# Kernel optimization log

Hardware: AMD Instinct MI355X
Metric: run time of the kernel (lower is better)

The kernel has to match this reference:

```python
import jax, jax.numpy as jnp
import numpy as np

B, S_T, S_S, P, D = 4, 8, 4, 1024, 1024
NUM_REF = 256
NUM_SHARED = 256
TOPK = 4
TEMP = 1.0
STUDENT_FRAMES = [0, 2, 4, 6]          # teacher indices used by student
EXTRA_FRAMES = [1, 3, 5, 7]            # teacher-only frames
SHARED_TEACHER = [2, 4, 6]             # shared frames (student_frame_indices[1:])
W_D1 = W_D2 = W_D3 = 1.0
HUBER_OUTER_BETA = 0.5


def setup_inputs() -> dict:
    key = jax.random.key(0)
    k1, k2, k3, k4 = jax.random.split(key, 4)
    teacher_feats = jax.random.normal(k1, (B, S_T, P, D), dtype=jnp.float32)
    student_feats = jax.random.normal(k2, (B, S_S, P, D), dtype=jnp.float32)
    ref_perm = jax.random.randint(k3, (NUM_REF,), 0, P, dtype=jnp.int32)
    shared_perm = jax.random.randint(k4, (NUM_SHARED,), 0, P, dtype=jnp.int32)
    return {"teacher_feats": teacher_feats, "student_feats": student_feats,
            "ref_perm": ref_perm, "shared_perm": shared_perm}


def _l2_normalize(x, eps=1e-12):
    n = jnp.maximum(jnp.linalg.norm(x, axis=-1, keepdims=True), eps)
    return x / n


def _smooth_l1_zero(x, beta):
    # SmoothL1Loss(x, 0) elementwise
    ax = jnp.abs(x)
    return jnp.where(ax < beta, 0.5 * ax * ax / beta, ax - 0.5 * beta)


def _kl_branch(diff_t, diff_s):
    # KL(softmax(diff_t/T) || softmax(diff_s/T)) over last dim, then outer huber vs 0
    log_p = jax.nn.log_softmax(diff_t / TEMP, axis=-1)
    log_q = jax.nn.log_softmax(diff_s / TEMP, axis=-1)
    kl = jnp.sum(jnp.exp(log_p) * (log_p - log_q), axis=-1)
    return jnp.sum(_smooth_l1_zero(kl, HUBER_OUTER_BETA)), kl.size


def reference(teacher_feats, student_feats, ref_perm, shared_perm):
    sg = jax.lax.stop_gradient
    N = min(NUM_REF, NUM_SHARED)

    # ref frame (teacher idx 0 -> student idx 0), subsampled patches
    ref_t = sg(teacher_feats[:, 0][:, ref_perm, :])          # [B, num_ref, D]
    ref_s = student_feats[:, 0][:, ref_perm, :]

    # teacher-only frames concatenated along patch dim: [B, 4*P, D]
    extra_t = sg(teacher_feats[:, jnp.array(EXTRA_FRAMES)].reshape(B, len(EXTRA_FRAMES) * P, D))

    # cosine-similarity top-k search (selection_mode='topk')
    sim = jnp.einsum('bnd,bmd->bnm', _l2_normalize(ref_t), _l2_normalize(extra_t))
    _, topk_idx = jax.lax.top_k(sim, TOPK)                    # [B, num_ref, topk]
    sim_high = jax.vmap(lambda e, i: e[i])(extra_t, topk_idx)  # [B, num_ref, topk, D]
    sim_high = sg(sim_high)

    rt = ref_t[:, :N, :]
    rs = ref_s[:, :N, :]
    sh = sim_high[:, :N, :, :]

    sum_d1 = jnp.float32(0.0); sum_d2 = jnp.float32(0.0); sum_d3 = jnp.float32(0.0)
    n_d1 = 0; n_d2 = 0; n_d3 = 0

    for t_idx in SHARED_TEACHER:
        s_idx = STUDENT_FRAMES.index(t_idx)
        st = sg(teacher_feats[:, t_idx][:, shared_perm[:N], :])   # [B, N, D]
        ss = student_feats[:, s_idx][:, shared_perm[:N], :]

        # d1: ref - shared
        l1, c1 = _kl_branch(rt - st, rs - ss)
        sum_d1 += l1; n_d1 += c1
        # d2: ref - sim_high
        l2, c2 = _kl_branch(rt[:, :, None, :] - sh, rs[:, :, None, :] - sh)
        sum_d2 += l2; n_d2 += c2
        # d3: shared - sim_high
        l3, c3 = _kl_branch(st[:, :, None, :] - sh, ss[:, :, None, :] - sh)
        sum_d3 += l3; n_d3 += c3

    loss = (W_D1 * sum_d1 / n_d1 + W_D2 * sum_d2 / n_d2 + W_D3 * sum_d3 / n_d3)
    return loss
```

## Files before the change

### kernel.cpp

```cpp
#include <hip/hip_runtime.h>
#include <hip/hip_bf16.h>
#include <math.h>

#define BATCH 4

typedef __bf16 bf16x8 __attribute__((ext_vector_type(8)));
typedef float f32x4 __attribute__((ext_vector_type(4)));

#define LDSTRIDE 40

__global__ __launch_bounds__(256) void convert_kernel(const float* __restrict__ teacher,
                                                      const int* __restrict__ ref_perm,
                                                      __bf16* __restrict__ Abf,
                                                      __bf16* __restrict__ Bbf,
                                                      float* __restrict__ invnorm,
                                                      float* __restrict__ acc) {
    int blk = blockIdx.x;
    int b = blk / 4352;
    int r = blk - b * 4352;
    int t = threadIdx.x;
    if (blk == 0 && t < 4) acc[t] = 0.f;
    const float* src;
    __bf16* dst;
    bool isB = (r >= 256);
    if (!isB) {
        src = teacher + (((size_t)b * 8 + 0) * 1024 + ref_perm[r]) * 1024;
        dst = Abf + ((size_t)b * 256 + r) * 1024;
    } else {
        int m = r - 256;
        int frame = 1 + 2 * (m >> 10), p = m & 1023;
        src = teacher + (((size_t)b * 8 + frame) * 1024 + p) * 1024;
        dst = Bbf + ((size_t)b * 4096 + m) * 1024;
    }
    float4 v = ((const float4*)src)[t];
    float scale = 1.0f;
    __shared__ float red[4];
    if (isB) {
        float s = v.x * v.x + v.y * v.y + v.z * v.z + v.w * v.w;
        for (int o = 32; o > 0; o >>= 1) s += __shfl_xor(s, o);
        if ((t & 63) == 0) red[t >> 6] = s;
        __syncthreads();
        float tot = red[0] + red[1] + red[2] + red[3];
        scale = 1.0f / fmaxf(sqrtf(tot), 1e-12f);
        if (t == 0) invnorm[b * 4096 + (r - 256)] = scale;
    }
    __bf16 o4[4] = {(__bf16)(v.x * scale), (__bf16)(v.y * scale),
                    (__bf16)(v.z * scale), (__bf16)(v.w * scale)};
    ((uint2*)dst)[t] = *(uint2*)o4;
}

__global__ __launch_bounds__(512) void mfma_gemm_kernel(const __bf16* __restrict__ Abf,
                                                        const __bf16* __restrict__ Bbf,
                                                        __bf16* __restrict__ scoresb) {
    int mt = blockIdx.x;
    int nt = blockIdx.y;
    int b  = blockIdx.z;
    int t = threadIdx.x;
    int lane = t & 63, wave = t >> 6;
    int wn0 = (wave & 1) * 64;
    int wm0 = (wave >> 1) * 32;
    int l15 = lane & 15, l4 = lane >> 4;

    __shared__ __bf16 As[128 * LDSTRIDE];
    __shared__ __bf16 Bs[128 * LDSTRIDE];

    const __bf16* Ab = Abf + ((size_t)b * 256 + nt * 128) * 1024;
    const __bf16* Bb = Bbf + ((size_t)b * 4096 + mt * 128) * 1024;

    int row0 = t >> 2, kc0 = t & 3;

    f32x4 acc[4][2] = {};

    for (int k0 = 0; k0 < 1024; k0 += 32) {
        uint4 a0 = *(const uint4*)(Ab + (size_t)row0 * 1024 + k0 + kc0 * 8);
        uint4 b0 = *(const uint4*)(Bb + (size_t)row0 * 1024 + k0 + kc0 * 8);
        __syncthreads();
        *(uint4*)(As + row0 * LDSTRIDE + kc0 * 8) = a0;
        *(uint4*)(Bs + row0 * LDSTRIDE + kc0 * 8) = b0;
        __syncthreads();
        bf16x8 af[4], bfr[2];
#pragma unroll
        for (int i = 0; i < 4; i++)
            af[i] = *(const bf16x8*)(As + (wn0 + i * 16 + l15) * LDSTRIDE + l4 * 8);
#pragma unroll
        for (int j = 0; j < 2; j++)
            bfr[j] = *(const bf16x8*)(Bs + (wm0 + j * 16 + l15) * LDSTRIDE + l4 * 8);
#pragma unroll
        for (int i = 0; i < 4; i++)
#pragma unroll
            for (int j = 0; j < 2; j++)
                acc[i][j] = __builtin_amdgcn_mfma_f32_16x16x32_bf16(af[i], bfr[j], acc[i][j], 0, 0, 0);
    }

    __bf16* outp = scoresb + ((size_t)b * 256 + nt * 128) * 4096 + (size_t)mt * 128;
#pragma unroll
    for (int i = 0; i < 4; i++)
#pragma unroll
        for (int j = 0; j < 2; j++)
#pragma unroll
            for (int r = 0; r < 4; r++) {
                int n = wn0 + i * 16 + l4 * 4 + r;
                int m = wm0 + j * 16 + l15;
                outp[(size_t)n * 4096 + m] = (__bf16)acc[i][j][r];
            }
}

__global__ __launch_bounds__(256) void topk_kl_kernel(const __bf16* __restrict__ scoresb,
                                                      const float* __restrict__ teacher,
                                                      const float* __restrict__ student,
                                                      const int* __restrict__ ref_perm,
                                                      const int* __restrict__ shared_perm,
                                                      const float* __restrict__ invnorm,
                                                      float* __restrict__ acc) {
    int row = blockIdx.x;
    int b = row >> 8, n = row & 255;
    int t = threadIdx.x;
    int lane = t & 63, wave = t >> 6;

    __shared__ float rt[1024], rs[1024], st[1024], ss[1024];
    __shared__ float sh8[8][1024];
    __shared__ float cval[32];
    __shared__ int cidx[32];
    __shared__ int cand_i[8];
    __shared__ float exact_v[8];
    __shared__ int wslot[4];
    __shared__ float res3[3];
    if (t < 3) res3[t] = 0.f;

    const float* Tb = teacher + (size_t)b * 8 * 1024 * 1024;
    const float* Sb = student + (size_t)b * 4 * 1024 * 1024;

    int rp = ref_perm[n];
    ((float4*)rt)[t] = ((const float4*)(Tb + (size_t)rp * 1024))[t];
    ((float4*)rs)[t] = ((const float4*)(Sb + (size_t)rp * 1024))[t];

    const __bf16* srow = scoresb + (size_t)row * 4096;
    __bf16 xs[16];
    *(uint4*)xs = ((const uint4*)srow)[2 * t];
    *(uint4*)(xs + 8) = ((const uint4*)srow)[2 * t + 1];

    float v[8]; int ix[8];
#pragma unroll
    for (int i = 0; i < 8; i++) { v[i] = -1e38f; ix[i] = -1; }
#pragma unroll
    for (int jj = 0; jj < 16; jj++) {
        float xv = (float)xs[jj]; int xm = t * 16 + jj;
        if (xv > v[7]) {
            v[7] = xv; ix[7] = xm;
#pragma unroll
            for (int i = 7; i > 0; i--)
                if (v[i] > v[i - 1]) {
                    float tv = v[i]; v[i] = v[i - 1]; v[i - 1] = tv;
                    int ti = ix[i]; ix[i] = ix[i - 1]; ix[i - 1] = ti;
                }
        }
    }
    for (int r = 0; r < 8; r++) {
        float bv = v[0]; int bi = ix[0];
        for (int o = 32; o > 0; o >>= 1) {
            float ov = __shfl_xor(bv, o); int oi = __shfl_xor(bi, o);
            if (ov > bv || (ov == bv && oi > bi)) { bv = ov; bi = oi; }
        }
        if (lane == 0) { cval[wave * 8 + r] = bv; cidx[wave * 8 + r] = bi; }
        if (bi == ix[0]) {
            v[0] = v[1]; ix[0] = ix[1];
            v[1] = v[2]; ix[1] = ix[2];
            v[2] = v[3]; ix[2] = ix[3];
            v[3] = v[4]; ix[3] = ix[4];
            v[4] = v[5]; ix[4] = ix[5];
            v[5] = v[6]; ix[5] = ix[6];
            v[6] = v[7]; ix[6] = ix[7];
            v[7] = -1e38f; ix[7] = -1;
        }
    }
    __syncthreads();
    if (wave == 0) {
        float mv = (lane < 32) ? cval[lane] : -1e38f;
        int mi = (lane < 32) ? cidx[lane] : -1;
        for (int r = 0; r < 8; r++) {
            float bv = mv; int bi = mi;
            for (int o = 32; o > 0; o >>= 1) {
                float ov = __shfl_xor(bv, o); int oi = __shfl_xor(bi, o);
                if (ov > bv || (ov == bv && oi > bi)) { bv = ov; bi = oi; }
            }
            if (lane == 0) cand_i[r] = bi;
            if (bi == mi) mv = -1e38f;
        }
    }
    __syncthreads();
#pragma unroll
    for (int c = 0; c < 8; c++) {
        int m = cand_i[c];
        int frame = 1 + 2 * (m >> 10), p = m & 1023;
        ((float4*)sh8[c])[t] = ((const float4*)(Tb + ((size_t)frame * 1024 + p) * 1024))[t];
    }
    __syncthreads();
    for (int c = wave; c < 8; c += 4) {
        float s = 0.f;
#pragma unroll
        for (int jj = 0; jj < 16; jj++) {
            int d = lane + 64 * jj;
            s = fmaf(rt[d], sh8[c][d], s);
        }
        for (int o = 32; o > 0; o >>= 1) s += __shfl_xor(s, o);
        if (lane == 0) exact_v[c] = s * invnorm[b * 4096 + cand_i[c]];
    }
    __syncthreads();
    if (t == 0) {
        unsigned used = 0;
        for (int r = 0; r < 4; r++) {
            float bv = -1e38f; int bc = 0;
            for (int c = 0; c < 8; c++)
                if (!(used & (1u << c)) && exact_v[c] > bv) { bv = exact_v[c]; bc = c; }
            used |= 1u << bc;
            wslot[r] = bc;
        }
    }
    __syncthreads();
    const float* shp[4] = {sh8[wslot[0]], sh8[wslot[1]], sh8[wslot[2]], sh8[wslot[3]]};

    int sp = shared_perm[n];
    for (int ti = 0; ti < 3; ti++) {
        int t_idx = 2 * ti + 2;
        int s_idx = ti + 1;
        __syncthreads();
        ((float4*)st)[t] = ((const float4*)(Tb + ((size_t)t_idx * 1024 + sp) * 1024))[t];
        ((float4*)ss)[t] = ((const float4*)(Sb + ((size_t)s_idx * 1024 + sp) * 1024))[t];
        __syncthreads();

        for (int r = wave; r < 9; r += 4) {
            const float *At, *Bt, *Asx, *Bsx;
            int branch;
            if (r == 0)      { At = rt; Bt = st;         Asx = rs; Bsx = ss;         branch = 0; }
            else if (r < 5)  { At = rt; Bt = shp[r - 1]; Asx = rs; Bsx = shp[r - 1]; branch = 1; }
            else             { At = st; Bt = shp[r - 5]; Asx = ss; Bsx = shp[r - 5]; branch = 2; }

            float dt[16], ds[16];
            float mt = -1e38f, ms = -1e38f;
#pragma unroll
            for (int j = 0; j < 16; j++) {
                int d = lane + 64 * j;
                dt[j] = At[d] - Bt[d];
                ds[j] = Asx[d] - Bsx[d];
                mt = fmaxf(mt, dt[j]);
                ms = fmaxf(ms, ds[j]);
            }
            for (int o = 32; o > 0; o >>= 1) {
                mt = fmaxf(mt, __shfl_xor(mt, o));
                ms = fmaxf(ms, __shfl_xor(ms, o));
            }
            float Zt = 0.f, Zs = 0.f, Tn = 0.f;
#pragma unroll
            for (int j = 0; j < 16; j++) {
                float et = __expf(dt[j] - mt);
                Zt += et;
                Zs += __expf(ds[j] - ms);
                Tn += et * (dt[j] - ds[j]);
            }
            for (int o = 32; o > 0; o >>= 1) {
                Zt += __shfl_xor(Zt, o);
                Zs += __shfl_xor(Zs, o);
                Tn += __shfl_xor(Tn, o);
            }
            if (lane == 0) {
                float kl = Tn / Zt - mt - __logf(Zt) + ms + __logf(Zs);
                float ax = fabsf(kl);
                float h = ax < 0.5f ? ax * ax : ax - 0.25f;
                atomicAdd(&res3[branch], h);
            }
        }
    }
    __syncthreads();
    if (t < 3) atomicAdd(&acc[t], res3[t]);
}

__global__ void finalize_kernel(const float* __restrict__ acc, float* __restrict__ out) {
    out[0] = acc[0] / 3072.f + acc[1] / 12288.f + acc[2] / 12288.f;
}

extern "C" void kernel_launch(void* const* d_in, const int* in_sizes, int n_in,
                              void* d_out, int out_size, void* d_ws, size_t ws_size,
                              hipStream_t stream) {
    const float* teacher = (const float*)d_in[0];
    const float* student = (const float*)d_in[1];
    const int* ref_perm = (const int*)d_in[2];
    const int* shared_perm = (const int*)d_in[3];
    float* out = (float*)d_out;

    char* ws = (char*)d_ws;
    float* acc     = (float*)ws;
    float* invnorm = (float*)(ws + 64);
    __bf16* Abf    = (__bf16*)(ws + 64 + 65536 + 16384);
    __bf16* Bbf    = Abf + (size_t)4 * 256 * 1024;
    __bf16* scoresb = Bbf + (size_t)4 * 4096 * 1024;

    convert_kernel<<<BATCH * 4352, 256, 0, stream>>>(teacher, ref_perm, Abf, Bbf, invnorm, acc);
    mfma_gemm_kernel<<<dim3(32, 2, 4), 512, 0, stream>>>(Abf, Bbf, scoresb);
    topk_kl_kernel<<<1024, 256, 0, stream>>>(scoresb, teacher, student, ref_perm, shared_perm, invnorm, acc);
    finalize_kernel<<<1, 1, 0, stream>>>(acc, out);
}
```

Before: 293.4 us.

## Split top-k rescoring and KL into separate kernels with per-frame grid

Splits the fused top-k/KL kernel into a rescoring kernel that writes top-4 indices to workspace, and a KL kernel launched over (row, shared frame) for three times more blocks. The d2 branch is computed once per row (in ti==0 blocks) and weighted by 3 because it does not depend on the shared frame. The rescoring step now reads candidate rows straight from global memory instead of staging all 8 in LDS. This shrinks LDS per block and raises parallelism, in exchange for an extra launch, reloading the ref and sim_high rows in every frame block, and uneven work across ti blocks.

```diff
diff --git a/kernel.cpp b/kernel.cpp
--- a/kernel.cpp
+++ b/kernel.cpp
@@ -105,34 +105,25 @@
             }
 }
 
-__global__ __launch_bounds__(256) void topk_kl_kernel(const __bf16* __restrict__ scoresb,
-                                                      const float* __restrict__ teacher,
-                                                      const float* __restrict__ student,
-                                                      const int* __restrict__ ref_perm,
-                                                      const int* __restrict__ shared_perm,
-                                                      const float* __restrict__ invnorm,
-                                                      float* __restrict__ acc) {
+__global__ __launch_bounds__(256) void topk_rescore_kernel(const __bf16* __restrict__ scoresb,
+                                                           const float* __restrict__ teacher,
+                                                           const int* __restrict__ ref_perm,
+                                                           const float* __restrict__ invnorm,
+                                                           int* __restrict__ topk) {
     int row = blockIdx.x;
     int b = row >> 8, n = row & 255;
     int t = threadIdx.x;
     int lane = t & 63, wave = t >> 6;
 
-    __shared__ float rt[1024], rs[1024], st[1024], ss[1024];
-    __shared__ float sh8[8][1024];
+    __shared__ float refr[1024];
     __shared__ float cval[32];
     __shared__ int cidx[32];
     __shared__ int cand_i[8];
     __shared__ float exact_v[8];
-    __shared__ int wslot[4];
-    __shared__ float res3[3];
-    if (t < 3) res3[t] = 0.f;
 
     const float* Tb = teacher + (size_t)b * 8 * 1024 * 1024;
-    const float* Sb = student + (size_t)b * 4 * 1024 * 1024;
-
     int rp = ref_perm[n];
-    ((float4*)rt)[t] = ((const float4*)(Tb + (size_t)rp * 1024))[t];
-    ((float4*)rs)[t] = ((const float4*)(Sb + (size_t)rp * 1024))[t];
+    ((float4*)refr)[t] = ((const float4*)(Tb + (size_t)rp * 1024))[t];
 
     const __bf16* srow = scoresb + (size_t)row * 4096;
     __bf16 xs[16];
@@ -188,22 +179,18 @@
         }
     }
     __syncthreads();
-#pragma unroll
-    for (int c = 0; c < 8; c++) {
+    for (int c = wave; c < 8; c += 4) {
         int m = cand_i[c];
         int frame = 1 + 2 * (m >> 10), p = m & 1023;
-        ((float4*)sh8[c])[t] = ((const float4*)(Tb + ((size_t)frame * 1024 + p) * 1024))[t];
-    }
-    __syncthreads();
-    for (int c = wave; c < 8; c += 4) {
+        const float* ext = Tb + ((size_t)frame * 1024 + p) * 1024;
         float s = 0.f;
 #pragma unroll
         for (int jj = 0; jj < 16; jj++) {
             int d = lane + 64 * jj;
-            s = fmaf(rt[d], sh8[c][d], s);
+            s = fmaf(refr[d], ext[d], s);
         }
         for (int o = 32; o > 0; o >>= 1) s += __shfl_xor(s, o);
-        if (lane == 0) exact_v[c] = s * invnorm[b * 4096 + cand_i[c]];
+        if (lane == 0) exact_v[c] = s * invnorm[b * 4096 + m];
     }
     __syncthreads();
     if (t == 0) {
@@ -213,61 +200,95 @@
             for (int c = 0; c < 8; c++)
                 if (!(used & (1u << c)) && exact_v[c] > bv) { bv = exact_v[c]; bc = c; }
             used |= 1u << bc;
-            wslot[r] = bc;
-        }
-    }
-    __syncthreads();
-    const float* shp[4] = {sh8[wslot[0]], sh8[wslot[1]], sh8[wslot[2]], sh8[wslot[3]]};
-
+            topk[row * 4 + r] = cand_i[bc];
+        }
+    }
+}
+
+#define RT 0
+#define RS 1024
+#define ST 2048
+#define SS 3072
+#define SH 4096
+__global__ __launch_bounds__(256) void kl_kernel(const float* __restrict__ teacher,
+                                                 const float* __restrict__ student,
+                                                 const int* __restrict__ ref_perm,
+                                                 const int* __restrict__ shared_perm,
+                                                 const int* __restrict__ topk,
+                                                 float* __restrict__ acc) {
+    int row = blockIdx.x;
+    int ti  = blockIdx.y;
+    int b = row >> 8;
+    int n = row & 255;
+    int t = threadIdx.x;
+    int lane = t & 63, wave = t >> 6;
+
+    __shared__ float buf[8192];
+    __shared__ float res3[3];
+    if (t < 3) res3[t] = 0.f;
+
+    const float* Tb = teacher + (size_t)b * 8 * 1024 * 1024;
+    const float* Sb = student + (size_t)b * 4 * 1024 * 1024;
+
+    int rp = ref_perm[n];
     int sp = shared_perm[n];
-    for (int ti = 0; ti < 3; ti++) {
-        int t_idx = 2 * ti + 2;
-        int s_idx = ti + 1;
-        __syncthreads();
-        ((float4*)st)[t] = ((const float4*)(Tb + ((size_t)t_idx * 1024 + sp) * 1024))[t];
-        ((float4*)ss)[t] = ((const float4*)(Sb + ((size_t)s_idx * 1024 + sp) * 1024))[t];
-        __syncthreads();
-
-        for (int r = wave; r < 9; r += 4) {
-            const float *At, *Bt, *Asx, *Bsx;
-            int branch;
-            if (r == 0)      { At = rt; Bt = st;         Asx = rs; Bsx = ss;         branch = 0; }
-            else if (r < 5)  { At = rt; Bt = shp[r - 1]; Asx = rs; Bsx = shp[r - 1]; branch = 1; }
-            else             { At = st; Bt = shp[r - 5]; Asx = ss; Bsx = shp[r - 5]; branch = 2; }
-
-            float dt[16], ds[16];
-            float mt = -1e38f, ms = -1e38f;
-#pragma unroll
-            for (int j = 0; j < 16; j++) {
-                int d = lane + 64 * j;
-                dt[j] = At[d] - Bt[d];
-                ds[j] = Asx[d] - Bsx[d];
-                mt = fmaxf(mt, dt[j]);
-                ms = fmaxf(ms, ds[j]);
-            }
-            for (int o = 32; o > 0; o >>= 1) {
-                mt = fmaxf(mt, __shfl_xor(mt, o));
-                ms = fmaxf(ms, __shfl_xor(ms, o));
-            }
-            float Zt = 0.f, Zs = 0.f, Tn = 0.f;
-#pragma unroll
-            for (int j = 0; j < 16; j++) {
-                float et = __expf(dt[j] - mt);
-                Zt += et;
-                Zs += __expf(ds[j] - ms);
-                Tn += et * (dt[j] - ds[j]);
-            }
-            for (int o = 32; o > 0; o >>= 1) {
-                Zt += __shfl_xor(Zt, o);
-                Zs += __shfl_xor(Zs, o);
-                Tn += __shfl_xor(Tn, o);
-            }
-            if (lane == 0) {
-                float kl = Tn / Zt - mt - __logf(Zt) + ms + __logf(Zs);
-                float ax = fabsf(kl);
-                float h = ax < 0.5f ? ax * ax : ax - 0.25f;
-                atomicAdd(&res3[branch], h);
-            }
+    int t_idx = 2 * ti + 2;
+    int s_idx = ti + 1;
+    ((float4*)(buf + RT))[t] = ((const float4*)(Tb + (size_t)rp * 1024))[t];
+    ((float4*)(buf + RS))[t] = ((const float4*)(Sb + (size_t)rp * 1024))[t];
+    ((float4*)(buf + ST))[t] = ((const float4*)(Tb + ((size_t)t_idx * 1024 + sp) * 1024))[t];
+    ((float4*)(buf + SS))[t] = ((const float4*)(Sb + ((size_t)s_idx * 1024 + sp) * 1024))[t];
+#pragma unroll
+    for (int k = 0; k < 4; k++) {
+        int idx = topk[row * 4 + k];
+        int frame = 1 + 2 * (idx >> 10), p = idx & 1023;
+        ((float4*)(buf + SH + k * 1024))[t] = ((const float4*)(Tb + ((size_t)frame * 1024 + p) * 1024))[t];
+    }
+    __syncthreads();
+
+    int nrows = (ti == 0) ? 9 : 5;
+    for (int idx = wave; idx < nrows; idx += 4) {
+        int r = (ti == 0) ? idx : (idx == 0 ? 0 : idx + 4);
+        int at, bt, as, bs, branch;
+        float w;
+        if (r == 0)      { at = RT; bt = ST;                 as = RS; bs = SS; branch = 0; w = 1.f; }
+        else if (r < 5)  { at = RT; bt = SH + (r - 1) * 1024; as = RS; bs = bt; branch = 1; w = 3.f; }
+        else             { at = ST; bt = SH + (r - 5) * 1024; as = SS; bs = bt; branch = 2; w = 1.f; }
+
+        float dt[16], ds[16];
+        float mt = -1e38f, ms = -1e38f;
+#pragma unroll
+        for (int j = 0; j < 16; j++) {
+            int d = lane + 64 * j;
+            float av = buf[at + d], bv = buf[bt + d];
+            float asv = buf[as + d], bsv = buf[bs + d];
+            dt[j] = av - bv;
+            ds[j] = asv - bsv;
+            mt = fmaxf(mt, dt[j]);
+            ms = fmaxf(ms, ds[j]);
+        }
+        for (int o = 32; o > 0; o >>= 1) {
+            mt = fmaxf(mt, __shfl_xor(mt, o));
+            ms = fmaxf(ms, __shfl_xor(ms, o));
+        }
+        float Zt = 0.f, Zs = 0.f, Tn = 0.f;
+#pragma unroll
+        for (int j = 0; j < 16; j++) {
+            float et = __expf(dt[j] - mt);
+            Zt += et;
+            Zs += __expf(ds[j] - ms);
+            Tn += et * (dt[j] - ds[j]);
+        }
+        for (int o = 32; o > 0; o >>= 1) {
+            Zt += __shfl_xor(Zt, o);
+            Zs += __shfl_xor(Zs, o);
+            Tn += __shfl_xor(Tn, o);
+        }
+        if (lane == 0) {
+            float kl = Tn / Zt - mt - __logf(Zt) + ms + __logf(Zs);
+            float ax = fabsf(kl);
+            float h = ax < 0.5f ? ax * ax : ax - 0.25f;
+            atomicAdd(&res3[branch], h * w);
         }
     }
     __syncthreads();
@@ -290,12 +311,14 @@
     char* ws = (char*)d_ws;
     float* acc     = (float*)ws;
     float* invnorm = (float*)(ws + 64);
+    int*   topk    = (int*)(ws + 64 + 65536);
     __bf16* Abf    = (__bf16*)(ws + 64 + 65536 + 16384);
     __bf16* Bbf    = Abf + (size_t)4 * 256 * 1024;
     __bf16* scoresb = Bbf + (size_t)4 * 4096 * 1024;
 
     convert_kernel<<<BATCH * 4352, 256, 0, stream>>>(teacher, ref_perm, Abf, Bbf, invnorm, acc);
     mfma_gemm_kernel<<<dim3(32, 2, 4), 512, 0, stream>>>(Abf, Bbf, scoresb);
-    topk_kl_kernel<<<1024, 256, 0, stream>>>(scoresb, teacher, student, ref_perm, shared_perm, invnorm, acc);
+    topk_rescore_kernel<<<1024, 256, 0, stream>>>(scoresb, teacher, ref_perm, invnorm, topk);
+    kl_kernel<<<dim3(1024, 3), 256, 0, stream>>>(teacher, student, ref_perm, shared_perm, topk, acc);
     finalize_kernel<<<1, 1, 0, stream>>>(acc, out);
 }
```

Result: no change. 293.9 us (+0.2%).
